# Kernel tuning notes

Hardware: AMD Instinct MI355X
Metric: run time of the kernel (lower is better)

Reference implementation:

```python
import jax, jax.numpy as jnp
import numpy as np
from jax import lax

B, C, H, W = 256, 3, 224, 224
M_MAG = 9.0  # RandAugment magnitude (init arg m)


def setup_inputs() -> dict:
    key = jax.random.key(0)
    k1, k2 = jax.random.split(key)
    # CIFAR-style normalization constants (as in the source module)
    mean = jnp.array([0.4914, 0.4822, 0.4465], dtype=jnp.float32)
    std = jnp.array([0.2023, 0.1994, 0.201], dtype=jnp.float32)
    # raw image in [0,1], then normalized (module expects normalized input)
    img = jax.random.uniform(k1, (B, C, H, W), dtype=jnp.float32)
    x = (img - mean[None, :, None, None]) / std[None, :, None, None]
    return {"x": x, "mean": mean, "std": std}


def _forward(x, mean, std):
    # deterministic op chain: sharpness -> contrast -> brightness -> solarize
    v_blend = M_MAG / 30.0 * (1.9 - 0.1) + 0.1   # 0.64 for sharpness/contrast/brightness
    v_sol = M_MAG / 30.0 * 1.0                    # 0.3 solarize threshold
    m_ = mean[None, :, None, None]
    s_ = std[None, :, None, None]

    # denormalize
    y = x * s_ + m_

    # sharpness: blend with 3x3 blur (kernel [[1,1,1],[1,5,1],[1,1,1]]/13, zero pad)
    k = jnp.array([[1., 1., 1.], [1., 5., 1.], [1., 1., 1.]], dtype=y.dtype) / 13.0
    kern = jnp.broadcast_to(k[None, None], (3, 1, 3, 3))  # depthwise OIHW
    blur = lax.conv_general_dilated(
        y, kern, window_strides=(1, 1), padding=[(1, 1), (1, 1)],
        feature_group_count=3, dimension_numbers=("NCHW", "OIHW", "NCHW"))
    y = y * v_blend + blur * (1.0 - v_blend)

    # contrast: blend with per-image mean of grayscale
    gray = 0.299 * y[:, 0] + 0.587 * y[:, 1] + 0.114 * y[:, 2]  # [B,H,W]
    gm = gray.mean(axis=(1, 2))[:, None, None, None]             # [B,1,1,1]
    y = y * v_blend + gm * (1.0 - v_blend)

    # brightness: blend with zeros
    y = y * v_blend

    # solarize: invert pixels >= threshold
    y = jnp.where(y < v_sol, y, 1.0 - y)

    # normalize
    return (y - m_) / s_


def reference(x, mean, std):
    return _forward(x, mean, std)
```

## Files before the change

kernel.cpp:

```cpp
#include <hip/hip_runtime.h>

#define IMG_B 256
#define IMG_H 224
#define IMG_W 224
#define HWPIX 50176
#define YP 228

#define FA(a,b) __fadd_rn((a),(b))
#define FM(a,b) __fmul_rn((a),(b))
#define FS(a,b) __fsub_rn((a),(b))
#define FD(a,b) __fdiv_rn((a),(b))

__device__ __forceinline__ float VBF()   { return (float)(9.0/30.0*(1.9-0.1)+0.1); }
__device__ __forceinline__ float OMVBF() { return (float)(1.0 - (9.0/30.0*(1.9-0.1)+0.1)); }
__device__ __forceinline__ float VSF()   { return (float)(9.0/30.0*1.0); }

__device__ __forceinline__ void y1_from_rows(const float* yU, const float* yC,
                                             const float* yD, float* y1o) {
    const float WN = 1.0f / 13.0f, WC = 5.0f / 13.0f;
#pragma unroll
    for (int mm = 0; mm < 4; ++mm) {
        float acc = 0.0f;
        acc = FA(acc, FM(WN, yU[mm + 0]));
        acc = FA(acc, FM(WN, yU[mm + 1]));
        acc = FA(acc, FM(WN, yU[mm + 2]));
        acc = FA(acc, FM(WN, yC[mm + 0]));
        acc = FA(acc, FM(WC, yC[mm + 1]));
        acc = FA(acc, FM(WN, yC[mm + 2]));
        acc = FA(acc, FM(WN, yD[mm + 0]));
        acc = FA(acc, FM(WN, yD[mm + 1]));
        acc = FA(acc, FM(WN, yD[mm + 2]));
        y1o[mm] = FA(FM(yC[mm + 1], VBF()), FM(acc, OMVBF()));
    }
}

__device__ __forceinline__ void stage_load(const float* __restrict__ xc, int r0,
                                           int t, float4* pf) {
#pragma unroll
    for (int u = 0; u < 4; ++u) {
        const int idx = t + 256 * u;
        float4 v = make_float4(0.f, 0.f, 0.f, 0.f);
        if (idx < 896) {
            const int row = idx / 56, c4 = (idx % 56) * 4;
            const int gi = r0 - 1 + row;
            if (gi >= 0 && gi < IMG_H)
                v = *(const float4*)(xc + (size_t)gi * IMG_W + c4);
        }
        pf[u] = v;
    }
}

__device__ __forceinline__ void stage_write(float s, float m, int r0, int t,
                                            const float4* pf, float* __restrict__ Y,
                                            int P) {
#pragma unroll
    for (int u = 0; u < 4; ++u) {
        const int idx = t + 256 * u;
        if (idx < 896) {
            const int row = idx / 56, c4 = (idx % 56) * 4;
            const int gi = r0 - 1 + row;
            float4 w;
            if (gi >= 0 && gi < IMG_H) {
                w.x = FA(FM(pf[u].x, s), m);
                w.y = FA(FM(pf[u].y, s), m);
                w.z = FA(FM(pf[u].z, s), m);
                w.w = FA(FM(pf[u].w, s), m);
            } else {
                w.x = w.y = w.z = w.w = 0.0f;
            }
            *(float4*)(&Y[row * P + c4]) = w;
        }
    }
}

__device__ __forceinline__ void lds_y6(const float* __restrict__ r, int j, float* y6) {
    const float4 vC = *(const float4*)(r + j);
    const float4 vL = *(const float4*)(r + (j > 0 ? j - 4 : 0));
    const float4 vR = *(const float4*)(r + (j + 4 < IMG_W ? j + 4 : IMG_W - 4));
    y6[0] = (j > 0) ? vL.w : 0.0f;
    y6[1] = vC.x; y6[2] = vC.y; y6[3] = vC.z; y6[4] = vC.w;
    y6[5] = (j + 4 < IMG_W) ? vR.x : 0.0f;
}

__global__ __launch_bounds__(256, 4) void kA1(const float* __restrict__ x,
                                              const float* __restrict__ mean_,
                                              const float* __restrict__ std_,
                                              float* __restrict__ part) {
    const int ck = blockIdx.x & 15, b = blockIdx.x >> 4;
    const int t = threadIdx.x;
    const int r0 = ck * 14;

    __shared__ float SM[3648];
    float* Y  = SM;
    float* G2 = SM;
    float* CH = SM + 3328;
    float* LS = SM + 3584;

    const float CGRAY[3] = {0.299f, 0.587f, 0.114f};

    const int rg  = t / 56;
    const int col = t - rg * 56;
    const bool active = (t < 224);
    const int rcount = (rg < 2) ? 4 : 3;
    const int rstart = (rg < 2) ? rg * 4 : 8 + (rg - 2) * 3;
    const int jd = col * 4;
    const bool lwave = ((t & 63) == 0)  && (col > 0);
    const bool rwave = ((t & 63) == 63) && (col < 55);

    float4 pf[4];
    float4 gacc[4];

#define LOADROW(V, LWv, RWv, yr) do {                                 \
        V   = *(const float4*)(&Y[(yr) * YP + jd]);                   \
        LWv = __shfl_up(V.w, 1, 64);                                  \
        RWv = __shfl_down(V.x, 1, 64);                                \
        if (lwave) LWv = Y[(yr) * YP + jd - 1];                       \
        if (rwave) RWv = Y[(yr) * YP + jd + 4];                       \
    } while (0)

#define FILL6(y6, V, LWv, RWv) do {                                   \
        y6[0] = (col > 0) ? LWv : 0.0f;                               \
        y6[1] = V.x; y6[2] = V.y; y6[3] = V.z; y6[4] = V.w;           \
        y6[5] = (col < 55) ? RWv : 0.0f;                              \
    } while (0)

    stage_load(x + (size_t)(b * 3 + 0) * HWPIX, r0, t, pf);

    for (int c = 0; c < 3; ++c) {
        stage_write(std_[c], mean_[c], r0, t, pf, Y, YP);
        __syncthreads();
        if (c < 2) stage_load(x + (size_t)(b * 3 + c + 1) * HWPIX, r0, t, pf);

        if (active) {
            const float cg = CGRAY[c];
            float4 v0, v1, v2;
            float la0, la1, la2, ra0, ra1, ra2;
            LOADROW(v0, la0, ra0, rstart);
            LOADROW(v1, la1, ra1, rstart + 1);
#pragma unroll
            for (int k = 0; k < 4; ++k) {
                if (k < rcount) {
                    LOADROW(v2, la2, ra2, rstart + k + 2);
                    float yU[6], yC[6], yD[6], y1[4];
                    FILL6(yU, v0, la0, ra0);
                    FILL6(yC, v1, la1, ra1);
                    FILL6(yD, v2, la2, ra2);
                    y1_from_rows(yU, yC, yD, y1);
                    float4 ga = gacc[k];
                    if (c == 0) {
                        ga.x = FM(cg, y1[0]); ga.y = FM(cg, y1[1]);
                        ga.z = FM(cg, y1[2]); ga.w = FM(cg, y1[3]);
                    } else {
                        ga.x = FA(ga.x, FM(cg, y1[0])); ga.y = FA(ga.y, FM(cg, y1[1]));
                        ga.z = FA(ga.z, FM(cg, y1[2])); ga.w = FA(ga.w, FM(cg, y1[3]));
                    }
                    gacc[k] = ga;
                    v0 = v1; la0 = la1; ra0 = ra1;
                    v1 = v2; la1 = la2; ra1 = ra2;
                }
            }
        }
        __syncthreads();
    }

    if (active) {
#pragma unroll
        for (int k = 0; k < 4; ++k) {
            if (k < rcount) {
                const int pl = (rstart + k) * IMG_W + jd;
                const int grp = pl / 392;
                const int rem = pl - grp * 392;
                int li = rem / 96; if (li > 3) li = 3;
                const int o = rem - 96 * li;
                *(float4*)(&G2[(grp * 4 + li) * 104 + o]) = gacc[k];
            }
        }
    }
    __syncthreads();

    {
        const int leaf = t >> 3, e = t & 7;
        const int base = leaf * 104 + e;
        const int nk = ((leaf & 3) == 3) ? 13 : 12;
        float r = G2[base];
        for (int k = 1; k < nk; ++k) r = FA(r, G2[base + 8 * k]);
        CH[t] = r;
    }
    __syncthreads();

    if (t < 32) {
        const float* c8 = &CH[t * 8];
        LS[t] = FA(FA(FA(c8[0], c8[1]), FA(c8[2], c8[3])),
                   FA(FA(c8[4], c8[5]), FA(c8[6], c8[7])));
    }
    __syncthreads();

    if (t == 0) {
        float v[32];
#pragma unroll
        for (int k = 0; k < 32; ++k) v[k] = LS[k];
        for (int n = 16; n >= 1; n >>= 1)
            for (int k = 0; k < n; ++k) v[k] = FA(v[2 * k], v[2 * k + 1]);
        part[blockIdx.x] = v[0];
    }
#undef LOADROW
#undef FILL6
}

__global__ __launch_bounds__(256) void kB(const float* __restrict__ x,
                                          const float* __restrict__ mean_,
                                          const float* __restrict__ std_,
                                          const float* __restrict__ part,
                                          float* __restrict__ out) {
    const int ck = blockIdx.x, c = blockIdx.y, b = blockIdx.z;
    const int t = threadIdx.x;
    const int r0 = ck * 14;

    __shared__ float Y[16 * IMG_W];
    __shared__ float gsh;

    const float s = std_[c], m = mean_[c];
    float4 pf[4];
    stage_load(x + (size_t)(b * 3 + c) * HWPIX, r0, t, pf);
    stage_write(s, m, r0, t, pf, Y, IMG_W);

    if (t == 0) {
        float v[16];
#pragma unroll
        for (int k = 0; k < 16; ++k) v[k] = part[b * 16 + k];
#pragma unroll
        for (int n = 8; n >= 1; n >>= 1)
#pragma unroll
            for (int k = 0; k < 8; ++k)
                if (k < n) v[k] = FA(v[2 * k], v[2 * k + 1]);
        gsh = FD(v[0], 50176.0f);
    }
    __syncthreads();
    const float g = gsh;

    float* oc = out + (size_t)(b * 3 + c) * HWPIX + (size_t)r0 * IMG_W;

    for (int qi = t; qi < 784; qi += 256) {
        const int lr = qi / 56 + 1, j = (qi % 56) * 4;
        float yU[6], yC[6], yD[6], y1[4];
        lds_y6(&Y[(lr - 1) * IMG_W], j, yU);
        lds_y6(&Y[lr * IMG_W],       j, yC);
        lds_y6(&Y[(lr + 1) * IMG_W], j, yD);
        y1_from_rows(yU, yC, yD, y1);

        float ov[4];
#pragma unroll
        for (int mm = 0; mm < 4; ++mm) {
            const float y2 = FA(FM(y1[mm], VBF()), FM(g, OMVBF()));
            const float y3 = FM(y2, VBF());
            const float y4 = (y3 < VSF()) ? y3 : FS(1.0f, y3);
            ov[mm] = FD(FS(y4, m), s);
        }
        float4 o;
        o.x = ov[0]; o.y = ov[1]; o.z = ov[2]; o.w = ov[3];
        *(float4*)(oc + (size_t)(lr - 1) * IMG_W + j) = o;
    }
}

extern "C" void kernel_launch(void* const* d_in, const int* in_sizes, int n_in,
                              void* d_out, int out_size, void* d_ws, size_t ws_size,
                              hipStream_t stream) {
    const float* x     = (const float*)d_in[0];
    const float* mean_ = (const float*)d_in[1];
    const float* std_  = (const float*)d_in[2];
    float* out = (float*)d_out;

    float* part = (float*)d_ws;

    kA1<<<IMG_B * 16, 256, 0, stream>>>(x, mean_, std_, part);

    dim3 gridB(16, 3, IMG_B);
    kB<<<gridB, 256, 0, stream>>>(x, mean_, std_, part, out);
}
```

Measured before the change: 93.88 us.

## Load all three channels into LDS at once in kA1 and remap workgroups

kA1 used to stage one channel at a time through registers into LDS, with syncs between channels. It now loads all three channels' 16-row tiles into a larger LDS buffer up front, behind a single barrier, and computes the blurred grayscale from all three channels in one pass. It also drops the occupancy hint from launch_bounds and permutes the block index so consecutive blocks spread across XCDs. The larger LDS use (about 44KB) and extra registers may lower occupancy, and the loss of cross-channel load/compute overlap could offset the fewer barriers.

New measurement: 116.1 us. 23.7% more time.

```diff
diff --git a/kernel.cpp b/kernel.cpp
--- a/kernel.cpp
+++ b/kernel.cpp
@@ -82,21 +82,19 @@
     y6[5] = (j + 4 < IMG_W) ? vR.x : 0.0f;
 }
 
-__global__ __launch_bounds__(256, 4) void kA1(const float* __restrict__ x,
-                                              const float* __restrict__ mean_,
-                                              const float* __restrict__ std_,
-                                              float* __restrict__ part) {
-    const int ck = blockIdx.x & 15, b = blockIdx.x >> 4;
+__global__ __launch_bounds__(256) void kA1(const float* __restrict__ x,
+                                           const float* __restrict__ mean_,
+                                           const float* __restrict__ std_,
+                                           float* __restrict__ part) {
+    const int wg = (blockIdx.x & 7) * 512 + (blockIdx.x >> 3);
+    const int ck = wg & 15, b = wg >> 4;
     const int t = threadIdx.x;
     const int r0 = ck * 14;
 
-    __shared__ float SM[3648];
-    float* Y  = SM;
+    __shared__ float SM[3 * 16 * YP];
     float* G2 = SM;
     float* CH = SM + 3328;
     float* LS = SM + 3584;
-
-    const float CGRAY[3] = {0.299f, 0.587f, 0.114f};
 
     const int rg  = t / 56;
     const int col = t - rg * 56;
@@ -107,15 +105,45 @@
     const bool lwave = ((t & 63) == 0)  && (col > 0);
     const bool rwave = ((t & 63) == 63) && (col < 55);
 
-    float4 pf[4];
     float4 gacc[4];
 
-#define LOADROW(V, LWv, RWv, yr) do {                                 \
-        V   = *(const float4*)(&Y[(yr) * YP + jd]);                   \
+    const float s0 = std_[0], s1 = std_[1], s2 = std_[2];
+    const float m0 = mean_[0], m1 = mean_[1], m2 = mean_[2];
+
+    {
+        const float sv[3] = {s0, s1, s2};
+        const float mv[3] = {m0, m1, m2};
+        const float* xb = x + (size_t)b * 3 * HWPIX;
+#pragma unroll
+        for (int u = 0; u < 11; ++u) {
+            const int idx = t + 256 * u;
+            if (idx < 2688) {
+                const int chn = idx / 896;
+                const int rem = idx - chn * 896;
+                const int row = rem / 56, c4 = (rem % 56) * 4;
+                const int gi = r0 - 1 + row;
+                float4 w = make_float4(0.f, 0.f, 0.f, 0.f);
+                if (gi >= 0 && gi < IMG_H) {
+                    const float4 xv = *(const float4*)(xb + (size_t)chn * HWPIX
+                                                       + (size_t)gi * IMG_W + c4);
+                    const float s = sv[chn], m = mv[chn];
+                    w.x = FA(FM(xv.x, s), m);
+                    w.y = FA(FM(xv.y, s), m);
+                    w.z = FA(FM(xv.z, s), m);
+                    w.w = FA(FM(xv.w, s), m);
+                }
+                *(float4*)(&SM[(chn * 16 + row) * YP + c4]) = w;
+            }
+        }
+    }
+    __syncthreads();
+
+#define LOADROW(V, LWv, RWv, base, yr) do {                           \
+        V   = *(const float4*)(&SM[(base) + (yr) * YP + jd]);         \
         LWv = __shfl_up(V.w, 1, 64);                                  \
         RWv = __shfl_down(V.x, 1, 64);                                \
-        if (lwave) LWv = Y[(yr) * YP + jd - 1];                       \
-        if (rwave) RWv = Y[(yr) * YP + jd + 4];                       \
+        if (lwave) LWv = SM[(base) + (yr) * YP + jd - 1];             \
+        if (rwave) RWv = SM[(base) + (yr) * YP + jd + 4];             \
     } while (0)
 
 #define FILL6(y6, V, LWv, RWv) do {                                   \
@@ -124,44 +152,46 @@
         y6[5] = (col < 55) ? RWv : 0.0f;                              \
     } while (0)
 
-    stage_load(x + (size_t)(b * 3 + 0) * HWPIX, r0, t, pf);
-
-    for (int c = 0; c < 3; ++c) {
-        stage_write(std_[c], mean_[c], r0, t, pf, Y, YP);
-        __syncthreads();
-        if (c < 2) stage_load(x + (size_t)(b * 3 + c + 1) * HWPIX, r0, t, pf);
-
-        if (active) {
-            const float cg = CGRAY[c];
-            float4 v0, v1, v2;
-            float la0, la1, la2, ra0, ra1, ra2;
-            LOADROW(v0, la0, ra0, rstart);
-            LOADROW(v1, la1, ra1, rstart + 1);
-#pragma unroll
-            for (int k = 0; k < 4; ++k) {
-                if (k < rcount) {
-                    LOADROW(v2, la2, ra2, rstart + k + 2);
-                    float yU[6], yC[6], yD[6], y1[4];
-                    FILL6(yU, v0, la0, ra0);
-                    FILL6(yC, v1, la1, ra1);
-                    FILL6(yD, v2, la2, ra2);
-                    y1_from_rows(yU, yC, yD, y1);
-                    float4 ga = gacc[k];
-                    if (c == 0) {
-                        ga.x = FM(cg, y1[0]); ga.y = FM(cg, y1[1]);
-                        ga.z = FM(cg, y1[2]); ga.w = FM(cg, y1[3]);
-                    } else {
-                        ga.x = FA(ga.x, FM(cg, y1[0])); ga.y = FA(ga.y, FM(cg, y1[1]));
-                        ga.z = FA(ga.z, FM(cg, y1[2])); ga.w = FA(ga.w, FM(cg, y1[3]));
-                    }
-                    gacc[k] = ga;
-                    v0 = v1; la0 = la1; ra0 = ra1;
-                    v1 = v2; la1 = la2; ra1 = ra2;
-                }
+    if (active) {
+        const float C0 = 0.299f, C1 = 0.587f, C2 = 0.114f;
+        float4 a0, a1, a2, b0, b1, b2, c0, c1, c2;
+        float al0, al1, al2, ar0, ar1, ar2;
+        float bl0, bl1, bl2, br0, br1, br2;
+        float cl0, cl1, cl2, cr0, cr1, cr2;
+        const int baseA = 0, baseB = 16 * YP, baseC = 32 * YP;
+        LOADROW(a0, al0, ar0, baseA, rstart);
+        LOADROW(a1, al1, ar1, baseA, rstart + 1);
+        LOADROW(b0, bl0, br0, baseB, rstart);
+        LOADROW(b1, bl1, br1, baseB, rstart + 1);
+        LOADROW(c0, cl0, cr0, baseC, rstart);
+        LOADROW(c1, cl1, cr1, baseC, rstart + 1);
+#pragma unroll
+        for (int k = 0; k < 4; ++k) {
+            if (k < rcount) {
+                LOADROW(a2, al2, ar2, baseA, rstart + k + 2);
+                LOADROW(b2, bl2, br2, baseB, rstart + k + 2);
+                LOADROW(c2, cl2, cr2, baseC, rstart + k + 2);
+                float yU[6], yC[6], yD[6];
+                float y1a[4], y1b[4], y1c[4];
+                FILL6(yU, a0, al0, ar0); FILL6(yC, a1, al1, ar1); FILL6(yD, a2, al2, ar2);
+                y1_from_rows(yU, yC, yD, y1a);
+                FILL6(yU, b0, bl0, br0); FILL6(yC, b1, bl1, br1); FILL6(yD, b2, bl2, br2);
+                y1_from_rows(yU, yC, yD, y1b);
+                FILL6(yU, c0, cl0, cr0); FILL6(yC, c1, cl1, cr1); FILL6(yD, c2, cl2, cr2);
+                y1_from_rows(yU, yC, yD, y1c);
+                float4 ga;
+                ga.x = FA(FA(FM(C0, y1a[0]), FM(C1, y1b[0])), FM(C2, y1c[0]));
+                ga.y = FA(FA(FM(C0, y1a[1]), FM(C1, y1b[1])), FM(C2, y1c[1]));
+                ga.z = FA(FA(FM(C0, y1a[2]), FM(C1, y1b[2])), FM(C2, y1c[2]));
+                ga.w = FA(FA(FM(C0, y1a[3]), FM(C1, y1b[3])), FM(C2, y1c[3]));
+                gacc[k] = ga;
+                a0 = a1; al0 = al1; ar0 = ar1; a1 = a2; al1 = al2; ar1 = ar2;
+                b0 = b1; bl0 = bl1; br0 = br1; b1 = b2; bl1 = bl2; br1 = br2;
+                c0 = c1; cl0 = cl1; cr0 = cr1; c1 = c2; cl1 = cl2; cr1 = cr2;
             }
         }
-        __syncthreads();
-    }
+    }
+    __syncthreads();
 
     if (active) {
 #pragma unroll
@@ -201,7 +231,7 @@
         for (int k = 0; k < 32; ++k) v[k] = LS[k];
         for (int n = 16; n >= 1; n >>= 1)
             for (int k = 0; k < n; ++k) v[k] = FA(v[2 * k], v[2 * k + 1]);
-        part[blockIdx.x] = v[0];
+        part[wg] = v[0];
     }
 #undef LOADROW
 #undef FILL6
```

## Blur grayscale once instead of blurring each channel separately in mean pass

Applied to the files above, without the earlier changes.

The mean-reduction kernel now loads all three channels at once, forms the grayscale image in shared memory, and runs the 3x3 blur a single time. Before, it blurred each channel and accumulated weighted results over three staged passes. Because blur is linear, this cuts the stencil work and two block barriers to one pass. The floating-point summation order changes, so the per-image mean may differ slightly in rounding. It also raises register pressure from holding twelve float4 loads per thread.

Result: faster. 84.73 us (-9.7%).

```diff
diff --git a/kernel.cpp b/kernel.cpp
--- a/kernel.cpp
+++ b/kernel.cpp
@@ -96,8 +96,6 @@
     float* CH = SM + 3328;
     float* LS = SM + 3584;
 
-    const float CGRAY[3] = {0.299f, 0.587f, 0.114f};
-
     const int rg  = t / 56;
     const int col = t - rg * 56;
     const bool active = (t < 224);
@@ -107,8 +105,47 @@
     const bool lwave = ((t & 63) == 0)  && (col > 0);
     const bool rwave = ((t & 63) == 63) && (col < 55);
 
-    float4 pf[4];
-    float4 gacc[4];
+    const float s0 = std_[0], s1 = std_[1], s2 = std_[2];
+    const float m0 = mean_[0], m1 = mean_[1], m2 = mean_[2];
+    const float C0 = 0.299f, C1 = 0.587f, C2 = 0.114f;
+
+    float4 q0[4], q1[4], q2[4];
+#pragma unroll
+    for (int u = 0; u < 4; ++u) {
+        const int idx = t + 256 * u;
+        q0[u] = q1[u] = q2[u] = make_float4(0.f, 0.f, 0.f, 0.f);
+        if (idx < 896) {
+            const int row = idx / 56, c4 = (idx % 56) * 4;
+            const int gi = r0 - 1 + row;
+            if (gi >= 0 && gi < IMG_H) {
+                const float* p = x + (size_t)b * 3 * HWPIX + (size_t)gi * IMG_W + c4;
+                q0[u] = *(const float4*)(p);
+                q1[u] = *(const float4*)(p + HWPIX);
+                q2[u] = *(const float4*)(p + 2 * HWPIX);
+            }
+        }
+    }
+#define GRAY1(a0v, a1v, a2v)                                              \
+    FA(FA(FM(C0, FA(FM(a0v, s0), m0)), FM(C1, FA(FM(a1v, s1), m1))),      \
+       FM(C2, FA(FM(a2v, s2), m2)))
+#pragma unroll
+    for (int u = 0; u < 4; ++u) {
+        const int idx = t + 256 * u;
+        if (idx < 896) {
+            const int row = idx / 56, c4 = (idx % 56) * 4;
+            const int gi = r0 - 1 + row;
+            float4 w = make_float4(0.f, 0.f, 0.f, 0.f);
+            if (gi >= 0 && gi < IMG_H) {
+                w.x = GRAY1(q0[u].x, q1[u].x, q2[u].x);
+                w.y = GRAY1(q0[u].y, q1[u].y, q2[u].y);
+                w.z = GRAY1(q0[u].z, q1[u].z, q2[u].z);
+                w.w = GRAY1(q0[u].w, q1[u].w, q2[u].w);
+            }
+            *(float4*)(&Y[row * YP + c4]) = w;
+        }
+    }
+#undef GRAY1
+    __syncthreads();
 
 #define LOADROW(V, LWv, RWv, yr) do {                                 \
         V   = *(const float4*)(&Y[(yr) * YP + jd]);                   \
@@ -124,44 +161,30 @@
         y6[5] = (col < 55) ? RWv : 0.0f;                              \
     } while (0)
 
-    stage_load(x + (size_t)(b * 3 + 0) * HWPIX, r0, t, pf);
-
-    for (int c = 0; c < 3; ++c) {
-        stage_write(std_[c], mean_[c], r0, t, pf, Y, YP);
-        __syncthreads();
-        if (c < 2) stage_load(x + (size_t)(b * 3 + c + 1) * HWPIX, r0, t, pf);
-
-        if (active) {
-            const float cg = CGRAY[c];
-            float4 v0, v1, v2;
-            float la0, la1, la2, ra0, ra1, ra2;
-            LOADROW(v0, la0, ra0, rstart);
-            LOADROW(v1, la1, ra1, rstart + 1);
-#pragma unroll
-            for (int k = 0; k < 4; ++k) {
-                if (k < rcount) {
-                    LOADROW(v2, la2, ra2, rstart + k + 2);
-                    float yU[6], yC[6], yD[6], y1[4];
-                    FILL6(yU, v0, la0, ra0);
-                    FILL6(yC, v1, la1, ra1);
-                    FILL6(yD, v2, la2, ra2);
-                    y1_from_rows(yU, yC, yD, y1);
-                    float4 ga = gacc[k];
-                    if (c == 0) {
-                        ga.x = FM(cg, y1[0]); ga.y = FM(cg, y1[1]);
-                        ga.z = FM(cg, y1[2]); ga.w = FM(cg, y1[3]);
-                    } else {
-                        ga.x = FA(ga.x, FM(cg, y1[0])); ga.y = FA(ga.y, FM(cg, y1[1]));
-                        ga.z = FA(ga.z, FM(cg, y1[2])); ga.w = FA(ga.w, FM(cg, y1[3]));
-                    }
-                    gacc[k] = ga;
-                    v0 = v1; la0 = la1; ra0 = ra1;
-                    v1 = v2; la1 = la2; ra1 = ra2;
-                }
-            }
-        }
-        __syncthreads();
-    }
+    float4 gacc[4];
+
+    if (active) {
+        float4 v0, v1, v2;
+        float la0, la1, la2, ra0, ra1, ra2;
+        LOADROW(v0, la0, ra0, rstart);
+        LOADROW(v1, la1, ra1, rstart + 1);
+#pragma unroll
+        for (int k = 0; k < 4; ++k) {
+            if (k < rcount) {
+                LOADROW(v2, la2, ra2, rstart + k + 2);
+                float yU[6], yC[6], yD[6], y1g[4];
+                FILL6(yU, v0, la0, ra0);
+                FILL6(yC, v1, la1, ra1);
+                FILL6(yD, v2, la2, ra2);
+                y1_from_rows(yU, yC, yD, y1g);
+                gacc[k].x = y1g[0]; gacc[k].y = y1g[1];
+                gacc[k].z = y1g[2]; gacc[k].w = y1g[3];
+                v0 = v1; la0 = la1; ra0 = ra1;
+                v1 = v2; la1 = la2; ra1 = ra2;
+            }
+        }
+    }
+    __syncthreads();
 
     if (active) {
 #pragma unroll
```
